# Kernel optimization log

Hardware: AMD Instinct MI355X
Metric: run time of the kernel (lower is better)

Reference implementation:

```python
import jax, jax.numpy as jnp
import numpy as np

N_U, N_D = 64, 64
N_E = N_U + N_D
N_A = 32
N_SV, N_PV = 512, 64
# n1 = [4*N_A, N_SV, N_SV, N_SV]; n2 = [4, N_PV, N_PV, N_PV]


def setup_inputs() -> dict:
    key = jax.random.key(0)
    ks = jax.random.split(key, 32)
    n1 = [4 * N_A, N_SV, N_SV, N_SV]
    n2 = [4, N_PV, N_PV, N_PV]
    d = {}
    d['r'] = jax.random.normal(ks[0], (N_E, 3), jnp.float32)
    d['a'] = jax.random.normal(ks[1], (N_A, 3), jnp.float32)
    i = 2
    for l in range(3):
        fin = 3 * n1[l] + 2 * n2[l]
        d[f'V{l}_w'] = jax.random.normal(ks[i], (fin, n1[l + 1]), jnp.float32) / np.float32(np.sqrt(fin)); i += 1
        d[f'V{l}_b'] = jax.random.normal(ks[i], (n1[l + 1],), jnp.float32); i += 1
        d[f'W{l}_w'] = jax.random.normal(ks[i], (n2[l], n2[l + 1]), jnp.float32) / np.float32(np.sqrt(n2[l])); i += 1
        d[f'W{l}_b'] = jax.random.normal(ks[i], (n2[l + 1],), jnp.float32); i += 1
    fin = 3 * N_SV + 2 * N_PV
    d['after_w'] = jax.random.normal(ks[i], (fin, N_SV), jnp.float32) / np.float32(np.sqrt(fin)); i += 1
    d['after_b'] = jax.random.normal(ks[i], (N_SV,), jnp.float32); i += 1
    d['vhu_w'] = jax.random.normal(ks[i], (N_SV, N_SV // 2), jnp.float32) / np.float32(np.sqrt(N_SV)); i += 1
    d['vhu_b'] = jax.random.normal(ks[i], (N_SV // 2,), jnp.float32); i += 1
    d['vhd_w'] = jax.random.normal(ks[i], (N_SV, N_SV // 2), jnp.float32) / np.float32(np.sqrt(N_SV)); i += 1
    d['vhd_b'] = jax.random.normal(ks[i], (N_SV // 2,), jnp.float32); i += 1
    d['wu_w'] = jax.random.normal(ks[i], (N_SV // 2, N_U), jnp.float32) / np.float32(np.sqrt(N_SV // 2)); i += 1
    d['wu_b'] = jax.random.normal(ks[i], (N_U,), jnp.float32); i += 1
    d['wd_w'] = jax.random.normal(ks[i], (N_SV // 2, N_D), jnp.float32) / np.float32(np.sqrt(N_SV // 2)); i += 1
    d['wd_b'] = jax.random.normal(ks[i], (N_D,), jnp.float32); i += 1
    return d


def _fb_block(s_v, p_v):
    # s_v: (N_E, f_s), p_v: (N_E, N_E, f_p)
    s_u_mean = jnp.tile(s_v[:N_U].mean(0)[None, :], (N_E, 1))
    s_d_mean = jnp.tile(s_v[N_U:].mean(0)[None, :], (N_E, 1))
    p_u_mean = p_v[:N_U].mean(0)  # (N_E, f_p)
    p_d_mean = p_v[N_U:].mean(0)
    return jnp.concatenate([s_u_mean, s_d_mean, p_u_mean, p_d_mean, s_v], axis=-1)


def _forward(r, a, Vw, Vb, Ww, Wb, after_w, after_b, vhu_w, vhu_b, vhd_w, vhd_b, wu_w, wu_b, wd_w, wd_b):
    eye = jnp.eye(N_E, dtype=r.dtype)[:, :, None]
    ra = r[:, None, :] - a[None, :, :]                       # (N_E, N_A, 3)
    ra_len = jnp.linalg.norm(ra, axis=-1, keepdims=True)     # (N_E, N_A, 1)
    rr = r[None, :, :] - r[:, None, :]                       # (N_E, N_E, 3)
    rr_len = jnp.linalg.norm(rr + eye, axis=-1, keepdims=True) * (1.0 - eye)
    s_v = jnp.concatenate([ra, ra_len], axis=-1).reshape(N_E, -1)  # (N_E, 4*N_A)
    p_v = jnp.concatenate([rr, rr_len], axis=-1)                   # (N_E, N_E, 4)
    for vw, vb, ww, wb in zip(Vw, Vb, Ww, Wb):
        s_in = _fb_block(s_v, p_v)
        # NOTE: torch residual `s_v if s_v.shape[-1]==n_sv` never fires here:
        # fb_block output width is 3*n1+2*n2 != n_sv, so it adds zeros.
        s_v = jnp.tanh(s_in @ vw + vb)
        p_new = jnp.tanh(p_v @ ww + wb)
        p_v = p_new + (p_v if p_v.shape[-1] == N_PV else 0.0)
    s_in = _fb_block(s_v, p_v)
    s_v = jnp.tanh(s_in @ after_w + after_b)  # (N_E, N_SV); residual again never fires
    s_u = s_v[:N_U] @ vhu_w + vhu_b
    s_d = s_v[N_U:] @ vhd_w + vhd_b
    s_wu = s_u @ wu_w + wu_b   # (N_U, N_U)
    s_wd = s_d @ wd_w + wd_b   # (N_D, N_D)
    exp_u = jnp.linalg.norm(ra[:N_U], axis=-1, keepdims=True)  # (N_U, N_A, 1)
    exp_d = jnp.linalg.norm(ra[N_U:], axis=-1, keepdims=True)
    orb_u = (s_wu * jnp.exp(-exp_u).sum(axis=1))[None]  # (1, N_U, N_U)
    orb_d = (s_wd * jnp.exp(-exp_d).sum(axis=1))[None]
    # logabssumdet for two (1,n,n) matrices with n>1: no 1x1 dets.
    sgn_u, ld_u = jnp.linalg.slogdet(orb_u)
    sgn_d, ld_d = jnp.linalg.slogdet(orb_d)
    sign = sgn_u * sgn_d
    logdet = ld_u + ld_d        # (1,)
    maxlogdet = logdet.max()
    psi = (sign * jnp.exp(logdet - maxlogdet)).sum()
    return jnp.log(jnp.abs(psi)) + maxlogdet  # scalar log|psi|


def reference(r, a, V0_w, V0_b, V1_w, V1_b, V2_w, V2_b, W0_w, W0_b, W1_w, W1_b, W2_w, W2_b,
              after_w, after_b, vhu_w, vhu_b, vhd_w, vhd_b, wu_w, wu_b, wd_w, wd_b):
    Vw, Vb = [V0_w, V1_w, V2_w], [V0_b, V1_b, V2_b]
    Ww, Wb = [W0_w, W1_w, W2_w], [W0_b, W1_b, W2_b]
    return _forward(r, a, Vw, Vb, Ww, Wb, after_w, after_b,
                    vhu_w, vhu_b, vhd_w, vhd_b, wu_w, wu_b, wd_w, wd_b)
```

## Files before the change

### kernel.cpp

```cpp
#include <hip/hip_runtime.h>
#include <math.h>

#define NSV 512

__global__ __launch_bounds__(512)
void pchain_kernel(const float* __restrict__ r, const float* __restrict__ apos,
                   const float* __restrict__ W0w, const float* __restrict__ W0b,
                   const float* __restrict__ W1w, const float* __restrict__ W1b,
                   const float* __restrict__ W2w, const float* __restrict__ W2b,
                   float* __restrict__ sv0, float* __restrict__ expv,
                   float* __restrict__ pme0, float* __restrict__ pme1,
                   float* __restrict__ pme2, float* __restrict__ pme3)
{
    __shared__ __align__(16) float sh[9472];
    float* rL    = sh;
    float* W0l   = sh + 384;
    float* aposL = sh + 640;
    float* shex  = sh + 736;
    float* p0c   = sh + 768;
    float* PA    = sh + 1024;
    float* Wbuf  = sh + 5376;
    const int b  = blockIdx.x;
    const int j  = b >> 1, sp = b & 1;
    const int t  = threadIdx.x;
    const int i  = t >> 3;
    const int o0 = (t & 7) * 8;

    if (t < 384) rL[t] = r[t];
    else if (t < 480) aposL[t - 384] = apos[t - 384];
    for (int idx = t; idx < 4096; idx += 512) Wbuf[idx] = W1w[idx];
    if (t < 256) W0l[t] = W0w[t];
    __syncthreads();

    const float rjx = rL[j*3+0], rjy = rL[j*3+1], rjz = rL[j*3+2];
    if (t < 64) {
        const int ii = sp*64 + t;
        float dx = rjx - rL[ii*3+0], dy = rjy - rL[ii*3+1], dz = rjz - rL[ii*3+2];
        float len = (ii == j) ? 0.f : sqrtf(dx*dx + dy*dy + dz*dz);
        p0c[t*4+0]=dx; p0c[t*4+1]=dy; p0c[t*4+2]=dz; p0c[t*4+3]=len;
    } else if (sp == 0 && t < 96) {
        const int k = t - 64;
        float dx = rjx - aposL[k*3+0], dy = rjy - aposL[k*3+1], dz = rjz - aposL[k*3+2];
        float len = sqrtf(dx*dx + dy*dy + dz*dz);
        float* spp = sv0 + (size_t)j*128 + k*4;
        spp[0]=dx; spp[1]=dy; spp[2]=dz; spp[3]=len;
        shex[k] = expf(-len);
    }
    __syncthreads();

    {
        const float x0=p0c[i*4+0], x1=p0c[i*4+1], x2=p0c[i*4+2], x3=p0c[i*4+3];
        #pragma unroll
        for (int k = 0; k < 8; ++k) {
            const int o = o0 + k;
            float a = W0b[o];
            a = fmaf(x0, W0l[o],     a);
            a = fmaf(x1, W0l[64+o],  a);
            a = fmaf(x2, W0l[128+o], a);
            a = fmaf(x3, W0l[192+o], a);
            PA[i*68+o] = tanhf(a);
        }
    }
    if (t < 4) {
        float s = 0.f;
        #pragma unroll 8
        for (int k = 0; k < 64; ++k) s += p0c[k*4 + t];
        pme0[j*8 + sp*4 + t] = s * 0.015625f;
    }
    if (sp == 0 && t == 4) {
        float s = 0.f;
        #pragma unroll 8
        for (int k = 0; k < 32; ++k) s += shex[k];
        expv[j] = s;
    }
    __syncthreads();

    if (t < 64) {
        float s = 0.f;
        #pragma unroll 8
        for (int k = 0; k < 64; ++k) s += PA[k*68 + t];
        pme1[j*128 + sp*64 + t] = s * 0.015625f;
    }
    float acc[8], res[8];
    const float* pa = PA + i*68;
    {
        #pragma unroll
        for (int k = 0; k < 8; ++k) acc[k] = W1b[o0+k];
        #pragma unroll 4
        for (int c = 0; c < 64; ++c) {
            const float av = pa[c];
            const float* wr = Wbuf + c*64 + o0;
            float4 wa = *reinterpret_cast<const float4*>(wr);
            float4 wb = *reinterpret_cast<const float4*>(wr+4);
            acc[0]=fmaf(av,wa.x,acc[0]); acc[1]=fmaf(av,wa.y,acc[1]);
            acc[2]=fmaf(av,wa.z,acc[2]); acc[3]=fmaf(av,wa.w,acc[3]);
            acc[4]=fmaf(av,wb.x,acc[4]); acc[5]=fmaf(av,wb.y,acc[5]);
            acc[6]=fmaf(av,wb.z,acc[6]); acc[7]=fmaf(av,wb.w,acc[7]);
        }
        #pragma unroll
        for (int k = 0; k < 8; ++k) res[k] = pa[o0+k];
    }
    __syncthreads();
    #pragma unroll
    for (int k = 0; k < 8; ++k) PA[i*68+o0+k] = tanhf(acc[k]) + res[k];
    __syncthreads();

    if (t < 64) {
        float s = 0.f;
        #pragma unroll 8
        for (int k = 0; k < 64; ++k) s += PA[k*68 + t];
        pme2[j*128 + sp*64 + t] = s * 0.015625f;
    }
    for (int idx = t; idx < 4096; idx += 512) Wbuf[idx] = W2w[idx];
    __syncthreads();

    {
        #pragma unroll
        for (int k = 0; k < 8; ++k) acc[k] = W2b[o0+k];
        #pragma unroll 4
        for (int c = 0; c < 64; ++c) {
            const float av = pa[c];
            const float* wr = Wbuf + c*64 + o0;
            float4 wa = *reinterpret_cast<const float4*>(wr);
            float4 wb = *reinterpret_cast<const float4*>(wr+4);
            acc[0]=fmaf(av,wa.x,acc[0]); acc[1]=fmaf(av,wa.y,acc[1]);
            acc[2]=fmaf(av,wa.z,acc[2]); acc[3]=fmaf(av,wa.w,acc[3]);
            acc[4]=fmaf(av,wb.x,acc[4]); acc[5]=fmaf(av,wb.y,acc[5]);
            acc[6]=fmaf(av,wb.z,acc[6]); acc[7]=fmaf(av,wb.w,acc[7]);
        }
        #pragma unroll
        for (int k = 0; k < 8; ++k) res[k] = pa[o0+k];
    }
    __syncthreads();
    #pragma unroll
    for (int k = 0; k < 8; ++k) PA[i*68+o0+k] = tanhf(acc[k]) + res[k];
    __syncthreads();

    if (t < 64) {
        float s = 0.f;
        #pragma unroll 8
        for (int k = 0; k < 64; ++k) s += PA[k*68 + t];
        pme3[j*128 + sp*64 + t] = s * 0.015625f;
    }
}

template<int FS, int FP, bool GEOM>
__global__ __launch_bounds__(512)
void a2_kernel(const float* __restrict__ svIn, const float* __restrict__ pmeIn,
               const float* __restrict__ psumIn,
               const float* __restrict__ r, const float* __restrict__ apos,
               const float* __restrict__ Vw, const float* __restrict__ Vb,
               float* __restrict__ svOut, float* __restrict__ psumOut)
{
    constexpr int KP  = 2*FP + FS;
    constexpr int KP2 = KP/2;
    __shared__ __align__(16) float As[4*KP];
    __shared__ __align__(16) float smL[2*FS];
    __shared__ __align__(16) float red[512];
    __shared__ float t1L[64];
    __shared__ float rL[384];
    __shared__ float aposL[96];
    const int t  = threadIdx.x;
    const int et = blockIdx.x >> 3;
    const int e0 = et * 4;
    const int o0 = (blockIdx.x & 7) * 64;
    const int ol = t & 63;
    const int o  = o0 + ol;
    const int wv = t >> 6;

    for (int idx = t; idx < 4*2*FP; idx += 512)
        As[(idx/(2*FP))*KP + idx%(2*FP)] =
            pmeIn[(size_t)(e0 + idx/(2*FP))*(2*FP) + idx%(2*FP)];
    for (int idx = t; idx < FS; idx += 512) {
        const int row = idx / (FS/4), c4 = idx % (FS/4);
        *reinterpret_cast<float4*>(&As[row*KP + 2*FP + c4*4]) =
            *reinterpret_cast<const float4*>(&svIn[(size_t)(e0+row)*FS + c4*4]);
    }
    if (GEOM) {
        if (t < 384) rL[t] = r[t];
        else if (t < 480) aposL[t - 384] = apos[t - 384];
        __syncthreads();
        {
            const int out = t >> 1, half = t & 1;
            const int spin = out >> 7, cc = out & 127, a_i = cc >> 2, d = cc & 3;
            const float ax = aposL[a_i*3+0], ay = aposL[a_i*3+1], az = aposL[a_i*3+2];
            float s = 0.f;
            #pragma unroll 8
            for (int q = 0; q < 32; ++q) {
                const int e = spin*64 + half*32 + q;
                float dx = rL[e*3+0]-ax, dy = rL[e*3+1]-ay, dz = rL[e*3+2]-az;
                float len = sqrtf(dx*dx + dy*dy + dz*dz);
                s += (d==0)?dx:(d==1)?dy:(d==2)?dz:len;
            }
            red[t] = s;
        }
        __syncthreads();
        if (t < 256) smL[t] = (red[2*t] + red[2*t+1]) * 0.015625f;
    } else {
        for (int idx = t; idx < 2*FS; idx += 512) {
            const int col = (idx < FS) ? idx : idx - FS;
            const int r0  = (idx < FS) ? 0 : 16;
            const float* base = psumIn + (size_t)r0*NSV + col;
            float s = 0.f;
            #pragma unroll
            for (int k = 0; k < 16; ++k) s += base[(size_t)k*NSV];
            smL[idx] = s * 0.015625f;
        }
    }
    __syncthreads();

    {
        constexpr int TI = (2*FS)/8;
        float a1 = 0.f;
        const float* Wp = Vw + (size_t)(wv*TI)*NSV + o;
        const float* mp = smL + wv*TI;
        #pragma unroll 8
        for (int k = 0; k < TI; ++k) a1 = fmaf(mp[k], Wp[(size_t)k*NSV], a1);
        red[wv*64 + ol] = a1;
    }
    __syncthreads();
    if (t < 64) {
        float s = Vb[o0 + t];
        #pragma unroll
        for (int g = 0; g < 8; ++g) s += red[g*64 + t];
        t1L[t] = s;
    }
    __syncthreads();

    const int e_l = wv & 3, kh = wv >> 2;
    {
        float a2 = (kh == 0) ? t1L[ol] : 0.f;
        const float* Ap = As + e_l*KP + kh*KP2;
        const float* Wp = Vw + (size_t)(2*FS + kh*KP2)*NSV + o;
        #pragma unroll 16
        for (int k = 0; k < KP2; ++k)
            a2 = fmaf(Ap[k], Wp[(size_t)k*NSV], a2);
        red[wv*64 + ol] = a2;
    }
    __syncthreads();
    float v = 0.f;
    if (t < 256) {
        v = tanhf(red[(t>>6)*64 + (t&63)] + red[((t>>6)+4)*64 + (t&63)]);
        svOut[(size_t)(e0 + (t>>6))*NSV + o0 + (t&63)] = v;
    }
    if (psumOut) {
        __syncthreads();
        if (t < 256) red[t] = v;
        __syncthreads();
        if (t < 64) {
            float s = red[t] + red[64+t] + red[128+t] + red[192+t];
            psumOut[(size_t)et*NSV + o0 + t] = s;
        }
    }
}

__global__ __launch_bounds__(512)
void headsw_kernel(const float* __restrict__ svF,
                   const float* __restrict__ vhu_w, const float* __restrict__ vhu_b,
                   const float* __restrict__ vhd_w, const float* __restrict__ vhd_b,
                   const float* __restrict__ wu_w,  const float* __restrict__ wu_b,
                   const float* __restrict__ wd_w,  const float* __restrict__ wd_b,
                   const float* __restrict__ expv,  float* __restrict__ orb)
{
    __shared__ __align__(16) float row[512];
    __shared__ __align__(16) float redH[512];
    __shared__ __align__(16) float tmpL[256];
    const int e = blockIdx.x;
    const int spin = e >> 6;
    const int t = threadIdx.x;
    row[t] = svF[(size_t)e*NSV + t];
    __syncthreads();

    const float* W1 = spin ? vhd_w : vhu_w;
    const float* B1 = spin ? vhd_b : vhu_b;
    {
        const int o = t & 255, kc = t >> 8;
        float acc = kc ? 0.f : B1[o];
        const float* Wp = W1 + (size_t)(kc*256)*256 + o;
        const float* rp = row + kc*256;
        #pragma unroll 8
        for (int f = 0; f < 256; ++f)
            acc = fmaf(rp[f], Wp[(size_t)f*256], acc);
        redH[t] = acc;
    }
    __syncthreads();
    if (t < 256) tmpL[t] = redH[t] + redH[256 + t];
    __syncthreads();

    const float* W2 = spin ? wd_w : wu_w;
    const float* B2 = spin ? wd_b : wu_b;
    {
        const int o = t & 63, kc = t >> 6;
        float acc = 0.f;
        const float* Wp = W2 + (size_t)(kc*32)*64 + o;
        const float* tp = tmpL + kc*32;
        #pragma unroll
        for (int f = 0; f < 32; ++f)
            acc = fmaf(tp[f], Wp[(size_t)f*64], acc);
        redH[kc*64 + o] = acc;
    }
    __syncthreads();
    if (t < 64) {
        float s = B2[t];
        #pragma unroll
        for (int g = 0; g < 8; ++g) s += redH[g*64 + t];
        orb[(size_t)e*64 + t] = s * expv[e];
    }
}

__device__ __forceinline__ int imax2(int a, int b) { return a > b ? a : b; }
__device__ __forceinline__ float readlane_f(float x, int lane) {
    return __int_as_float(__builtin_amdgcn_readlane(__float_as_int(x), lane));
}

__global__ __launch_bounds__(128)
void det_kernel(const float* __restrict__ orb, float* __restrict__ out)
{
    __shared__ float parts[2];
    const int t = threadIdx.x;
    const int w = t >> 6;
    const int lane = t & 63;
    const float* M = orb + (size_t)w*4096 + (size_t)lane*64;
    float rr[64];
    #pragma unroll
    for (int j = 0; j < 64; j += 4) {
        float4 v = *reinterpret_cast<const float4*>(M + j);
        rr[j]=v.x; rr[j+1]=v.y; rr[j+2]=v.z; rr[j+3]=v.w;
    }
    float pv_mine = 1.f;
    bool active = true;
    #pragma unroll
    for (int k = 0; k < 64; ++k) {
        int bits = (int)(__float_as_uint(rr[k]) & 0x7FFFFFC0u);
        int v = active ? (bits | lane) : lane;
        int tmp;
        tmp = __builtin_amdgcn_update_dpp(0, v, 0xB1,  0xF, 0xF, true); v = imax2(v, tmp);
        tmp = __builtin_amdgcn_update_dpp(0, v, 0x4E,  0xF, 0xF, true); v = imax2(v, tmp);
        tmp = __builtin_amdgcn_update_dpp(0, v, 0x141, 0xF, 0xF, true); v = imax2(v, tmp);
        tmp = __builtin_amdgcn_update_dpp(0, v, 0x140, 0xF, 0xF, true); v = imax2(v, tmp);
        tmp = __builtin_amdgcn_update_dpp(0, v, 0x142, 0xF, 0xF, true); v = imax2(v, tmp);
        tmp = __builtin_amdgcn_update_dpp(0, v, 0x143, 0xF, 0xF, true); v = imax2(v, tmp);
        const int idx = __builtin_amdgcn_readlane(v, 63) & 63;
        const float piv = readlane_f(rr[k], idx);
        pv_mine = (lane == k) ? piv : pv_mine;
        const float linv = __builtin_amdgcn_rcpf(piv);
        const float l = (active && lane != idx) ? rr[k]*linv : 0.f;
        if (lane == idx) active = false;
        #pragma unroll
        for (int j = k+1; j < 64; ++j)
            rr[j] = fmaf(-l, readlane_f(rr[j], idx), rr[j]);
    }
    float lg = logf(fabsf(pv_mine));
    #pragma unroll
    for (int off = 32; off; off >>= 1) lg += __shfl_down(lg, off);
    if (lane == 0) parts[w] = lg;
    __syncthreads();
    if (t == 0) out[0] = parts[0] + parts[1];
}

extern "C" void kernel_launch(void* const* d_in, const int* in_sizes, int n_in,
                              void* d_out, int out_size, void* d_ws, size_t ws_size,
                              hipStream_t stream)
{
    const float* r    = (const float*)d_in[0];
    const float* apos = (const float*)d_in[1];
    const float* V0w  = (const float*)d_in[2];
    const float* V0b  = (const float*)d_in[3];
    const float* W0w  = (const float*)d_in[4];
    const float* W0b  = (const float*)d_in[5];
    const float* V1w  = (const float*)d_in[6];
    const float* V1b  = (const float*)d_in[7];
    const float* W1w  = (const float*)d_in[8];
    const float* W1b  = (const float*)d_in[9];
    const float* V2w  = (const float*)d_in[10];
    const float* V2b  = (const float*)d_in[11];
    const float* W2w  = (const float*)d_in[12];
    const float* W2b  = (const float*)d_in[13];
    const float* afw  = (const float*)d_in[14];
    const float* afb  = (const float*)d_in[15];
    const float* vhuw = (const float*)d_in[16];
    const float* vhub = (const float*)d_in[17];
    const float* vhdw = (const float*)d_in[18];
    const float* vhdb = (const float*)d_in[19];
    const float* wuw  = (const float*)d_in[20];
    const float* wub  = (const float*)d_in[21];
    const float* wdw  = (const float*)d_in[22];
    const float* wdb  = (const float*)d_in[23];

    float* ws   = (float*)d_ws;
    float* sv0  = ws;
    float* svA  = sv0  + 16384;
    float* svB  = svA  + 65536;
    float* expv = svB  + 65536;
    float* pme0 = expv + 128;
    float* pme1 = pme0 + 1024;
    float* pme2 = pme1 + 16384;
    float* pme3 = pme2 + 16384;
    float* psA  = pme3 + 16384;
    float* psB  = psA  + 16384;
    float* orb  = psB  + 16384;

    pchain_kernel<<<256, 512, 0, stream>>>(r, apos, W0w, W0b, W1w, W1b, W2w, W2b,
                                           sv0, expv, pme0, pme1, pme2, pme3);
    a2_kernel<128, 4, true  ><<<256, 512, 0, stream>>>(sv0, pme0, nullptr, r, apos,
                                                       V0w, V0b, svA, psA);
    a2_kernel<512, 64, false><<<256, 512, 0, stream>>>(svA, pme1, psA, r, apos,
                                                       V1w, V1b, svB, psB);
    a2_kernel<512, 64, false><<<256, 512, 0, stream>>>(svB, pme2, psB, r, apos,
                                                       V2w, V2b, svA, psA);
    a2_kernel<512, 64, false><<<256, 512, 0, stream>>>(svA, pme3, psA, r, apos,
                                                       afw, afb, svB, nullptr);
    headsw_kernel<<<128, 512, 0, stream>>>(svB, vhuw, vhub, vhdw, vhdb,
                                           wuw, wub, wdw, wdb, expv, orb);
    det_kernel<<<1, 128, 0, stream>>>(orb, (float*)d_out);
}
```

Measured before the change: 105.5 us.

## Merge pair-chain and first FermiNet layer into one front kernel

The first a2 layer no longer reads from pchain outputs. It recomputes the electron-atom features and the pair means from positions on its own, so it can run concurrently with the pair-chain as extra blocks of a single 512-block launch. This removes one kernel launch and the serialization between pchain and layer 0, along with the sv0/pme0 workspace round trip. The cost is redundant geometry recomputation in each a0 block, and the a0 blocks now carry the larger shared-memory footprint of the merged kernel.

```diff
diff --git a/kernel.cpp b/kernel.cpp
--- a/kernel.cpp
+++ b/kernel.cpp
@@ -3,16 +3,15 @@
 
 #define NSV 512
 
-__global__ __launch_bounds__(512)
-void pchain_kernel(const float* __restrict__ r, const float* __restrict__ apos,
-                   const float* __restrict__ W0w, const float* __restrict__ W0b,
-                   const float* __restrict__ W1w, const float* __restrict__ W1b,
-                   const float* __restrict__ W2w, const float* __restrict__ W2b,
-                   float* __restrict__ sv0, float* __restrict__ expv,
-                   float* __restrict__ pme0, float* __restrict__ pme1,
-                   float* __restrict__ pme2, float* __restrict__ pme3)
-{
-    __shared__ __align__(16) float sh[9472];
+__device__ void pchain_role(int b, const float* __restrict__ r,
+                            const float* __restrict__ apos,
+                            const float* __restrict__ W0w, const float* __restrict__ W0b,
+                            const float* __restrict__ W1w, const float* __restrict__ W1b,
+                            const float* __restrict__ W2w, const float* __restrict__ W2b,
+                            float* __restrict__ expv,
+                            float* __restrict__ pme1, float* __restrict__ pme2,
+                            float* __restrict__ pme3, float* sh)
+{
     float* rL    = sh;
     float* W0l   = sh + 384;
     float* aposL = sh + 640;
@@ -20,7 +19,6 @@
     float* p0c   = sh + 768;
     float* PA    = sh + 1024;
     float* Wbuf  = sh + 5376;
-    const int b  = blockIdx.x;
     const int j  = b >> 1, sp = b & 1;
     const int t  = threadIdx.x;
     const int i  = t >> 3;
@@ -41,10 +39,7 @@
     } else if (sp == 0 && t < 96) {
         const int k = t - 64;
         float dx = rjx - aposL[k*3+0], dy = rjy - aposL[k*3+1], dz = rjz - aposL[k*3+2];
-        float len = sqrtf(dx*dx + dy*dy + dz*dz);
-        float* spp = sv0 + (size_t)j*128 + k*4;
-        spp[0]=dx; spp[1]=dy; spp[2]=dz; spp[3]=len;
-        shex[k] = expf(-len);
+        shex[k] = expf(-sqrtf(dx*dx + dy*dy + dz*dz));
     }
     __syncthreads();
 
@@ -60,12 +55,6 @@
             a = fmaf(x3, W0l[192+o], a);
             PA[i*68+o] = tanhf(a);
         }
-    }
-    if (t < 4) {
-        float s = 0.f;
-        #pragma unroll 8
-        for (int k = 0; k < 64; ++k) s += p0c[k*4 + t];
-        pme0[j*8 + sp*4 + t] = s * 0.015625f;
     }
     if (sp == 0 && t == 4) {
         float s = 0.f;
@@ -144,11 +133,135 @@
     }
 }
 
-template<int FS, int FP, bool GEOM>
+__device__ void a0_role(int ab, const float* __restrict__ r,
+                        const float* __restrict__ apos,
+                        const float* __restrict__ V0w, const float* __restrict__ V0b,
+                        float* __restrict__ svA, float* __restrict__ psA, float* sh)
+{
+    constexpr int KP = 136, KP2 = 68;
+    float* As    = sh;
+    float* smL   = sh + 544;
+    float* red   = sh + 800;
+    float* t1L   = sh + 1312;
+    float* rL    = sh + 1376;
+    float* aposL = sh + 1760;
+    const int t  = threadIdx.x;
+    const int et = ab >> 3, e0 = et * 4;
+    const int o0 = (ab & 7) * 64;
+    const int ol = t & 63, o = o0 + ol;
+    const int wv = t >> 6;
+
+    if (t < 384) rL[t] = r[t];
+    else if (t < 480) aposL[t - 384] = apos[t - 384];
+    __syncthreads();
+
+    if (t < 128) {
+        const int e_l = t >> 5, k = t & 31;
+        const int e = e0 + e_l;
+        float dx = rL[e*3+0]-aposL[k*3+0], dy = rL[e*3+1]-aposL[k*3+1],
+              dz = rL[e*3+2]-aposL[k*3+2];
+        float len = sqrtf(dx*dx + dy*dy + dz*dz);
+        float* dst = As + e_l*KP + 8 + k*4;
+        dst[0]=dx; dst[1]=dy; dst[2]=dz; dst[3]=len;
+    } else if (t < 160) {
+        const int q = t - 128;
+        const int e_l = q >> 3, outp = q & 7;
+        const int spin = outp >> 2, c = outp & 3;
+        const int e = e0 + e_l;
+        const float ex = rL[e*3+0], ey = rL[e*3+1], ez = rL[e*3+2];
+        float s = 0.f;
+        for (int i2 = 0; i2 < 64; ++i2) {
+            const int ii = spin*64 + i2;
+            float dx = ex - rL[ii*3+0], dy = ey - rL[ii*3+1], dz = ez - rL[ii*3+2];
+            float v = (c==0)?dx:(c==1)?dy:(c==2)?dz:
+                      ((ii==e)?0.f:sqrtf(dx*dx+dy*dy+dz*dz));
+            s += v;
+        }
+        As[e_l*KP + outp] = s * 0.015625f;
+    }
+    {
+        const int outp = t >> 1, half = t & 1;
+        const int spin = outp >> 7, cc = outp & 127, a_i = cc >> 2, d = cc & 3;
+        const float ax = aposL[a_i*3+0], ay = aposL[a_i*3+1], az = aposL[a_i*3+2];
+        float s = 0.f;
+        #pragma unroll 8
+        for (int q = 0; q < 32; ++q) {
+            const int e = spin*64 + half*32 + q;
+            float dx = rL[e*3+0]-ax, dy = rL[e*3+1]-ay, dz = rL[e*3+2]-az;
+            float len = sqrtf(dx*dx + dy*dy + dz*dz);
+            s += (d==0)?dx:(d==1)?dy:(d==2)?dz:len;
+        }
+        red[t] = s;
+    }
+    __syncthreads();
+    if (t < 256) smL[t] = (red[2*t] + red[2*t+1]) * 0.015625f;
+    __syncthreads();
+
+    {
+        float a1 = 0.f;
+        const float* Wp = V0w + (size_t)(wv*32)*NSV + o;
+        const float* mp = smL + wv*32;
+        #pragma unroll 8
+        for (int k = 0; k < 32; ++k) a1 = fmaf(mp[k], Wp[(size_t)k*NSV], a1);
+        red[wv*64 + ol] = a1;
+    }
+    __syncthreads();
+    if (t < 64) {
+        float s = V0b[o0 + t];
+        #pragma unroll
+        for (int g = 0; g < 8; ++g) s += red[g*64 + t];
+        t1L[t] = s;
+    }
+    __syncthreads();
+
+    const int e_l = wv & 3, kh = wv >> 2;
+    {
+        float a2 = (kh == 0) ? t1L[ol] : 0.f;
+        const float* Ap = As + e_l*KP + kh*KP2;
+        const float* Wp = V0w + (size_t)(256 + kh*KP2)*NSV + o;
+        #pragma unroll 16
+        for (int k = 0; k < KP2; ++k)
+            a2 = fmaf(Ap[k], Wp[(size_t)k*NSV], a2);
+        red[wv*64 + ol] = a2;
+    }
+    __syncthreads();
+    float v = 0.f;
+    if (t < 256) {
+        v = tanhf(red[(t>>6)*64 + (t&63)] + red[((t>>6)+4)*64 + (t&63)]);
+        svA[(size_t)(e0 + (t>>6))*NSV + o0 + (t&63)] = v;
+    }
+    __syncthreads();
+    if (t < 256) red[t] = v;
+    __syncthreads();
+    if (t < 64) {
+        float s = red[t] + red[64+t] + red[128+t] + red[192+t];
+        psA[(size_t)et*NSV + o0 + t] = s;
+    }
+}
+
+__global__ __launch_bounds__(512)
+void front_kernel(const float* __restrict__ r, const float* __restrict__ apos,
+                  const float* __restrict__ V0w, const float* __restrict__ V0b,
+                  const float* __restrict__ W0w, const float* __restrict__ W0b,
+                  const float* __restrict__ W1w, const float* __restrict__ W1b,
+                  const float* __restrict__ W2w, const float* __restrict__ W2b,
+                  float* __restrict__ svA, float* __restrict__ expv,
+                  float* __restrict__ pme1, float* __restrict__ pme2,
+                  float* __restrict__ pme3, float* __restrict__ psA)
+{
+    __shared__ __align__(16) float sh[9472];
+    const int b = blockIdx.x;
+    if (b < 256)
+        pchain_role(b, r, apos, W0w, W0b, W1w, W1b, W2w, W2b,
+                    expv, pme1, pme2, pme3, sh);
+    else
+        a0_role(b - 256, r, apos, V0w, V0b, svA, psA, sh);
+}
+
+template<int FS, int FP>
 __global__ __launch_bounds__(512)
 void a2_kernel(const float* __restrict__ svIn, const float* __restrict__ pmeIn,
                const float* __restrict__ psumIn,
-               const float* __restrict__ r, const float* __restrict__ apos,
                const float* __restrict__ Vw, const float* __restrict__ Vb,
                float* __restrict__ svOut, float* __restrict__ psumOut)
 {
@@ -158,8 +271,6 @@
     __shared__ __align__(16) float smL[2*FS];
     __shared__ __align__(16) float red[512];
     __shared__ float t1L[64];
-    __shared__ float rL[384];
-    __shared__ float aposL[96];
     const int t  = threadIdx.x;
     const int et = blockIdx.x >> 3;
     const int e0 = et * 4;
@@ -176,36 +287,14 @@
         *reinterpret_cast<float4*>(&As[row*KP + 2*FP + c4*4]) =
             *reinterpret_cast<const float4*>(&svIn[(size_t)(e0+row)*FS + c4*4]);
     }
-    if (GEOM) {
-        if (t < 384) rL[t] = r[t];
-        else if (t < 480) aposL[t - 384] = apos[t - 384];
-        __syncthreads();
-        {
-            const int out = t >> 1, half = t & 1;
-            const int spin = out >> 7, cc = out & 127, a_i = cc >> 2, d = cc & 3;
-            const float ax = aposL[a_i*3+0], ay = aposL[a_i*3+1], az = aposL[a_i*3+2];
-            float s = 0.f;
-            #pragma unroll 8
-            for (int q = 0; q < 32; ++q) {
-                const int e = spin*64 + half*32 + q;
-                float dx = rL[e*3+0]-ax, dy = rL[e*3+1]-ay, dz = rL[e*3+2]-az;
-                float len = sqrtf(dx*dx + dy*dy + dz*dz);
-                s += (d==0)?dx:(d==1)?dy:(d==2)?dz:len;
-            }
-            red[t] = s;
-        }
-        __syncthreads();
-        if (t < 256) smL[t] = (red[2*t] + red[2*t+1]) * 0.015625f;
-    } else {
-        for (int idx = t; idx < 2*FS; idx += 512) {
-            const int col = (idx < FS) ? idx : idx - FS;
-            const int r0  = (idx < FS) ? 0 : 16;
-            const float* base = psumIn + (size_t)r0*NSV + col;
-            float s = 0.f;
-            #pragma unroll
-            for (int k = 0; k < 16; ++k) s += base[(size_t)k*NSV];
-            smL[idx] = s * 0.015625f;
-        }
+    for (int idx = t; idx < 2*FS; idx += 512) {
+        const int col = (idx < FS) ? idx : idx - FS;
+        const int r0  = (idx < FS) ? 0 : 16;
+        const float* base = psumIn + (size_t)r0*NSV + col;
+        float s = 0.f;
+        #pragma unroll
+        for (int k = 0; k < 16; ++k) s += base[(size_t)k*NSV];
+        smL[idx] = s * 0.015625f;
     }
     __syncthreads();
 
@@ -388,28 +477,22 @@
     const float* wdb  = (const float*)d_in[23];
 
     float* ws   = (float*)d_ws;
-    float* sv0  = ws;
-    float* svA  = sv0  + 16384;
+    float* svA  = ws;
     float* svB  = svA  + 65536;
     float* expv = svB  + 65536;
-    float* pme0 = expv + 128;
-    float* pme1 = pme0 + 1024;
+    float* pme1 = expv + 128;
     float* pme2 = pme1 + 16384;
     float* pme3 = pme2 + 16384;
     float* psA  = pme3 + 16384;
     float* psB  = psA  + 16384;
     float* orb  = psB  + 16384;
 
-    pchain_kernel<<<256, 512, 0, stream>>>(r, apos, W0w, W0b, W1w, W1b, W2w, W2b,
-                                           sv0, expv, pme0, pme1, pme2, pme3);
-    a2_kernel<128, 4, true  ><<<256, 512, 0, stream>>>(sv0, pme0, nullptr, r, apos,
-                                                       V0w, V0b, svA, psA);
-    a2_kernel<512, 64, false><<<256, 512, 0, stream>>>(svA, pme1, psA, r, apos,
-                                                       V1w, V1b, svB, psB);
-    a2_kernel<512, 64, false><<<256, 512, 0, stream>>>(svB, pme2, psB, r, apos,
-                                                       V2w, V2b, svA, psA);
-    a2_kernel<512, 64, false><<<256, 512, 0, stream>>>(svA, pme3, psA, r, apos,
-                                                       afw, afb, svB, nullptr);
+    front_kernel<<<512, 512, 0, stream>>>(r, apos, V0w, V0b, W0w, W0b,
+                                          W1w, W1b, W2w, W2b,
+                                          svA, expv, pme1, pme2, pme3, psA);
+    a2_kernel<512, 64><<<256, 512, 0, stream>>>(svA, pme1, psA, V1w, V1b, svB, psB);
+    a2_kernel<512, 64><<<256, 512, 0, stream>>>(svB, pme2, psB, V2w, V2b, svA, psA);
+    a2_kernel<512, 64><<<256, 512, 0, stream>>>(svA, pme3, psA, afw, afb, svB, nullptr);
     headsw_kernel<<<128, 512, 0, stream>>>(svB, vhuw, vhub, vhdw, vhdb,
                                            wuw, wub, wdw, wdb, expv, orb);
     det_kernel<<<1, 128, 0, stream>>>(orb, (float*)d_out);
```

After: 101.7 us. 3.5% less time.
